# Kernel tuning notes

Hardware: AMD Instinct MI355X
Metric: run time of the kernel (lower is better)

Reference implementation:

```python
import jax, jax.numpy as jnp
import numpy as np

N_TOKENS = 8192
EMBED = 1024
HIDDEN = 4 * EMBED
NUM_EXPERTS = 8


def setup_inputs() -> dict:
    key = jax.random.key(0)
    ks = jax.random.split(key, 10)
    s = 0.02
    return {
        "x": jax.random.normal(ks[0], (N_TOKENS, EMBED), dtype=jnp.float32),
        # Router params
        "Wr1": jax.random.normal(ks[1], (EMBED, EMBED), dtype=jnp.float32) * s,
        "br1": jnp.zeros((EMBED,), dtype=jnp.float32),
        "Wr2": jax.random.normal(ks[2], (EMBED, NUM_EXPERTS), dtype=jnp.float32) * s,
        "br2": jnp.zeros((NUM_EXPERTS,), dtype=jnp.float32),
        # Expert FFN params, stacked over experts
        "W1": jax.random.normal(ks[3], (NUM_EXPERTS, EMBED, HIDDEN), dtype=jnp.float32) * s,
        "b1": jnp.zeros((NUM_EXPERTS, HIDDEN), dtype=jnp.float32),
        "W2": jax.random.normal(ks[4], (NUM_EXPERTS, HIDDEN, EMBED), dtype=jnp.float32) * s,
        "b2": jnp.zeros((NUM_EXPERTS, EMBED), dtype=jnp.float32),
    }


def reference(x, Wr1, br1, Wr2, br2, W1, b1, W2, b2):
    # Router: Linear -> ReLU -> Linear -> softmax over experts -> top-1
    h = jax.nn.relu(x @ Wr1 + br1)                      # [N, E]
    probs = jax.nn.softmax(h @ Wr2 + br2, axis=1)       # [N, num_experts]
    chosen = jnp.argmax(probs, axis=1)                  # [N]

    num_experts = W1.shape[0]
    out = jnp.zeros_like(x)
    # Fixed small loop over experts (structurally distinct weights).
    for e in range(num_experts):
        ffn_e = jax.nn.relu(x @ W1[e] + b1[e]) @ W2[e] + b2[e]  # [N, E]
        out = jnp.where((chosen == e)[:, None], ffn_e, out)
    # Note: original returns raw expert output (no probability weighting).
    return out
```

## Files before the change

kernel.cpp:

```cpp
#include <hip/hip_runtime.h>
#include <stdint.h>

#define N_TOK 8192
#define EMB 1024
#define HID 4096
#define NEXP 8

typedef _Float16 f16x8 __attribute__((ext_vector_type(8)));
typedef _Float16 f16x4 __attribute__((ext_vector_type(4)));
typedef short    s16x8 __attribute__((ext_vector_type(8)));
typedef unsigned short u16x8 __attribute__((ext_vector_type(8)));
typedef float    f32x4 __attribute__((ext_vector_type(4)));

typedef __attribute__((address_space(1))) const void gvoid_t;
typedef __attribute__((address_space(3))) void lvoid_t;

__device__ __forceinline__ void async16(const void* g, void* l) {
  __builtin_amdgcn_global_load_lds((gvoid_t*)g, (lvoid_t*)l, 16, 0, 0);
}

__device__ __forceinline__ unsigned short f2bf(float f) {
  unsigned u = __builtin_bit_cast(unsigned, f);
  u += 0x7fffu + ((u >> 16) & 1u);
  return (unsigned short)(u >> 16);
}

__global__ __launch_bounds__(256) void k_cast_x(const float* __restrict__ x,
    unsigned short* __restrict__ xb, _Float16* __restrict__ xhi, _Float16* __restrict__ xlo) {
  int i = (blockIdx.x * 256 + threadIdx.x) << 2;
  float4 v = *(const float4*)(x + i);
  ushort4 b;
  b.x = f2bf(v.x); b.y = f2bf(v.y); b.z = f2bf(v.z); b.w = f2bf(v.w);
  *(ushort4*)(xb + i) = b;
  float vv[4] = {v.x, v.y, v.z, v.w};
  f16x4 hi, lo;
#pragma unroll
  for (int j = 0; j < 4; j++) {
    _Float16 h = (_Float16)vv[j];
    hi[j] = h;
    lo[j] = (_Float16)(vv[j] - (float)h);
  }
  *(f16x4*)(xhi + i) = hi;
  *(f16x4*)(xlo + i) = lo;
}

__global__ __launch_bounds__(256) void k_trans_wr1(const float* __restrict__ src,
    _Float16* __restrict__ dhi, _Float16* __restrict__ dlo) {
  int nblk = blockIdx.x >> 4, kc = blockIdx.x & 15;
  int n = (nblk << 8) + threadIdx.x;
  int k0 = kc << 6;
  for (int k = k0; k < k0 + 64; k += 8) {
    f16x8 hi, lo;
#pragma unroll
    for (int j = 0; j < 8; j++) {
      float w = src[(size_t)(k + j) * EMB + n] * 256.0f;
      _Float16 h = (_Float16)w;
      hi[j] = h;
      lo[j] = (_Float16)(w - (float)h);
    }
    *(f16x8*)(dhi + (size_t)n * EMB + k) = hi;
    *(f16x8*)(dlo + (size_t)n * EMB + k) = lo;
  }
}

__global__ __launch_bounds__(256) void k_transcast_v2(const float* __restrict__ src,
    unsigned short* __restrict__ dst, int K, int Nn, int ktiles, int ntiles) {
  __shared__ __align__(16) unsigned short lds[256 * 72];
  int b = blockIdx.x;
  int e = b / (ktiles * ntiles);
  int r = b % (ktiles * ntiles);
  int kt = r / ntiles, nt = r % ntiles;
  int k0 = kt << 6, n0 = nt << 8;
  const float* s = src + (size_t)e * K * Nn;
  unsigned short* d = dst + (size_t)e * K * Nn;
  int tid = threadIdx.x;
  const float* scol = s + n0 + tid;
#pragma unroll 4
  for (int k = 0; k < 64; k += 2) {
    float a  = scol[(size_t)(k0 + k) * Nn];
    float bv = scol[(size_t)(k0 + k + 1) * Nn];
    unsigned p = (unsigned)f2bf(a) | ((unsigned)f2bf(bv) << 16);
    *(unsigned*)(lds + tid * 72 + k) = p;
  }
  __syncthreads();
  int c = tid & 7, nl = tid >> 3;
#pragma unroll
  for (int p2 = 0; p2 < 8; p2++) {
    int n = (p2 << 5) + nl;
    u16x8 v = *(const u16x8*)(lds + n * 72 + (c << 3));
    *(u16x8*)(d + (size_t)(n0 + n) * K + k0 + (c << 3)) = v;
  }
}

__global__ __launch_bounds__(256) void k_router_gemm(
    const _Float16* __restrict__ Ah, const _Float16* __restrict__ Al,
    const _Float16* __restrict__ Bh, const _Float16* __restrict__ Bl,
    const float* __restrict__ br1, float* __restrict__ hOut) {
  __shared__ __align__(16) _Float16 sAh[4096], sAl[4096], sBh[4096], sBl[4096];
  const int tid = threadIdx.x, lane = tid & 63, wave = tid >> 6;
  const int m0 = (blockIdx.x >> 3) << 7;
  const int n0 = (blockIdx.x & 7) << 7;
  const int srow = (wave << 5) + (lane >> 2);
  const int scol = (lane & 3) << 3;
  const size_t aBase = (size_t)(m0 + srow) * EMB + scol;
  const size_t bBase = (size_t)(n0 + srow) * EMB + scol;
  _Float16* lAh = sAh + (wave << 10);
  _Float16* lAl = sAl + (wave << 10);
  _Float16* lBh = sBh + (wave << 10);
  _Float16* lBl = sBl + (wave << 10);
  const int q = lane >> 4, c = lane & 15;
  const int msub = (wave & 1) << 6, nsub = (wave >> 1) << 6;
  f32x4 acc[4][4];
#pragma unroll
  for (int i = 0; i < 4; i++)
#pragma unroll
    for (int j = 0; j < 4; j++) acc[i][j] = (f32x4){0.f, 0.f, 0.f, 0.f};

  for (int kk = 0; kk < EMB; kk += 32) {
    async16(Ah + aBase + kk, lAh);
    async16(Ah + aBase + 16 * EMB + kk, lAh + 512);
    async16(Al + aBase + kk, lAl);
    async16(Al + aBase + 16 * EMB + kk, lAl + 512);
    async16(Bh + bBase + kk, lBh);
    async16(Bh + bBase + 16 * EMB + kk, lBh + 512);
    async16(Bl + bBase + kk, lBl);
    async16(Bl + bBase + 16 * EMB + kk, lBl + 512);
    __syncthreads();
    f16x8 fah[4], fal[4], fbh[4], fbl[4];
#pragma unroll
    for (int i = 0; i < 4; i++) {
      int ar = msub + (i << 4) + c;
      int br = nsub + (i << 4) + c;
      fah[i] = *(const f16x8*)(sAh + (ar << 5) + (q << 3));
      fal[i] = *(const f16x8*)(sAl + (ar << 5) + (q << 3));
      fbh[i] = *(const f16x8*)(sBh + (br << 5) + (q << 3));
      fbl[i] = *(const f16x8*)(sBl + (br << 5) + (q << 3));
    }
#pragma unroll
    for (int mi = 0; mi < 4; mi++)
#pragma unroll
      for (int ni = 0; ni < 4; ni++) {
        acc[mi][ni] = __builtin_amdgcn_mfma_f32_16x16x32_f16(fah[mi], fbh[ni], acc[mi][ni], 0, 0, 0);
        acc[mi][ni] = __builtin_amdgcn_mfma_f32_16x16x32_f16(fah[mi], fbl[ni], acc[mi][ni], 0, 0, 0);
        acc[mi][ni] = __builtin_amdgcn_mfma_f32_16x16x32_f16(fal[mi], fbh[ni], acc[mi][ni], 0, 0, 0);
      }
    __syncthreads();
  }
#pragma unroll
  for (int mi = 0; mi < 4; mi++)
#pragma unroll
    for (int ni = 0; ni < 4; ni++) {
      int gn = n0 + nsub + (ni << 4) + c;
      float bias = 256.0f * br1[gn];
#pragma unroll
      for (int i2 = 0; i2 < 4; i2++) {
        int gm = m0 + msub + (mi << 4) + (q << 2) + i2;
        float v = acc[mi][ni][i2] + bias;
        hOut[(size_t)gm * EMB + gn] = v > 0.f ? v : 0.f;
      }
    }
}

__global__ __launch_bounds__(256) void k_logits(const float* __restrict__ h,
    const float* __restrict__ Wr2, const float* __restrict__ br2, int* __restrict__ chosen) {
  __shared__ __align__(16) float sW[EMB * NEXP];
  int tid = threadIdx.x;
  for (int i = tid; i < EMB * NEXP; i += 256) sW[i] = Wr2[i];
  __syncthreads();
  int lane = tid & 63, wave = tid >> 6;
  int t = blockIdx.x * 4 + wave;
  const float* hr = h + (size_t)t * EMB;
  float acc[8] = {0.f, 0.f, 0.f, 0.f, 0.f, 0.f, 0.f, 0.f};
#pragma unroll
  for (int i = 0; i < 16; i++) {
    int k = (i << 6) + lane;
    float v = hr[k];
    float4 w0 = *(const float4*)(sW + (k << 3));
    float4 w1 = *(const float4*)(sW + (k << 3) + 4);
    acc[0] += v * w0.x; acc[1] += v * w0.y; acc[2] += v * w0.z; acc[3] += v * w0.w;
    acc[4] += v * w1.x; acc[5] += v * w1.y; acc[6] += v * w1.z; acc[7] += v * w1.w;
  }
#pragma unroll
  for (int off = 32; off > 0; off >>= 1)
#pragma unroll
    for (int e = 0; e < 8; e++) acc[e] += __shfl_down(acc[e], off);
  if (lane == 0) {
    float best = acc[0] + 256.0f * br2[0];
    int bi = 0;
#pragma unroll
    for (int e = 1; e < 8; e++) {
      float l = acc[e] + 256.0f * br2[e];
      if (l > best) { best = l; bi = e; }
    }
    chosen[t] = bi;
  }
}

__global__ void k_zero(int* meta) { meta[threadIdx.x] = 0; }

__global__ __launch_bounds__(256) void k_hist(const int* __restrict__ chosen, int* meta) {
  int i = blockIdx.x * 256 + threadIdx.x;
  atomicAdd(&meta[chosen[i]], 1);
}

__global__ __launch_bounds__(128) void k_sched(int* meta) {
  __shared__ int cnt[8];
  int tid = threadIdx.x;
  if (tid < 8) cnt[tid] = meta[tid];
  __syncthreads();
  int off[9]; off[0] = 0;
#pragma unroll
  for (int e = 0; e < 8; e++) off[e + 1] = off[e] + cnt[e];
  if (tid < 8) meta[16 + tid] = off[tid];
  int ts[9]; ts[0] = 0;
#pragma unroll
  for (int e = 0; e < 8; e++) ts[e + 1] = ts[e] + ((cnt[e] + 127) >> 7);
  int T = ts[8];
  if (tid == 0) { meta[24] = off[8]; meta[25] = T; }
  if (tid < T) {
    int e = 0;
    while (ts[e + 1] <= tid) e++;
    int m = off[e] + ((tid - ts[e]) << 7);
    int end = off[e + 1];
    meta[32 + tid] = e;
    meta[112 + tid] = m;
    meta[192 + tid] = (m + 128 < end) ? m + 128 : end;
  }
  int ts2[9]; ts2[0] = 0;
#pragma unroll
  for (int e = 0; e < 8; e++) ts2[e + 1] = ts2[e] + ((cnt[e] + 255) >> 8);
  int T2 = ts2[8];
  if (tid == 0) meta[26] = T2;
  if (tid < T2) {
    int e = 0;
    while (ts2[e + 1] <= tid) e++;
    int m = off[e] + ((tid - ts2[e]) << 8);
    int end = off[e + 1];
    meta[288 + tid] = e;
    meta[368 + tid] = m;
    meta[448 + tid] = (m + 256 < end) ? m + 256 : end;
  }
}

__global__ __launch_bounds__(256) void k_scatter(const int* __restrict__ chosen,
                                                 int* meta, int* __restrict__ perm) {
  int i = blockIdx.x * 256 + threadIdx.x;
  int e = chosen[i];
  int pos = meta[16 + e] + atomicAdd(&meta[8 + e], 1);
  perm[pos] = i;
}

__global__ __launch_bounds__(512) void k_ffn1(
    const unsigned short* __restrict__ xb, const unsigned short* __restrict__ w1t,
    const float* __restrict__ b1, const int* __restrict__ perm,
    const int* __restrict__ meta, unsigned short* __restrict__ hidden) {
  const int wg = (blockIdx.x & 7) * 160 + (blockIdx.x >> 3);
  const int mt = wg >> 5;
  if (mt >= meta[26]) return;
  const int nt = wg & 31;
  const int e = meta[288 + mt];
  const int row0 = meta[368 + mt];
  const int rend = meta[448 + mt];
  const int n0 = nt << 7;
  __shared__ __align__(16) unsigned short sA[256 * 64], sB[128 * 64];
  const int tid = threadIdx.x, lane = tid & 63, wave = tid >> 6;
  const int lr = lane >> 3;
  const int scol = ((lane & 7) ^ lr) << 3;
  const unsigned short* aptr[4];
#pragma unroll
  for (int j = 0; j < 4; j++) {
    int r = row0 + (wave << 5) + (j << 3) + lr;
    if (r > N_TOK - 1) r = N_TOK - 1;
    aptr[j] = xb + (size_t)perm[r] * EMB + scol;
  }
  const unsigned short* bptr[2];
#pragma unroll
  for (int j = 0; j < 2; j++) {
    int r = n0 + (wave << 4) + (j << 3) + lr;
    bptr[j] = w1t + (size_t)e * EMB * HID + (size_t)r * EMB + scol;
  }
  const int q = lane >> 4, c = lane & 15;
  const int msub = (wave >> 1) << 6;
  const int nsub = (wave & 1) << 6;
  f32x4 acc[4][4];
#pragma unroll
  for (int i = 0; i < 4; i++)
#pragma unroll
    for (int j = 0; j < 4; j++) acc[i][j] = (f32x4){0.f, 0.f, 0.f, 0.f};

#pragma unroll 1
  for (int kk = 0; kk < EMB; kk += 64) {
    async16(aptr[0] + kk, sA + ((wave << 5) + 0)  * 64);
    async16(aptr[1] + kk, sA + ((wave << 5) + 8)  * 64);
    async16(aptr[2] + kk, sA + ((wave << 5) + 16) * 64);
    async16(aptr[3] + kk, sA + ((wave << 5) + 24) * 64);
    async16(bptr[0] + kk, sB + ((wave << 4) + 0)  * 64);
    async16(bptr[1] + kk, sB + ((wave << 4) + 8)  * 64);
    __syncthreads();
#pragma unroll
    for (int ks = 0; ks < 2; ks++) {
      const int coff = ((((ks << 2) + q) ^ (c & 7)) << 3);
      s16x8 fa[4], fb[4];
#pragma unroll
      for (int i = 0; i < 4; i++) {
        fa[i] = *(const s16x8*)(sA + ((msub + (i << 4) + c) << 6) + coff);
        fb[i] = *(const s16x8*)(sB + ((nsub + (i << 4) + c) << 6) + coff);
      }
#pragma unroll
      for (int mi = 0; mi < 4; mi++)
#pragma unroll
        for (int ni = 0; ni < 4; ni++)
          acc[mi][ni] = __builtin_amdgcn_mfma_f32_16x16x32_bf16(fa[mi], fb[ni], acc[mi][ni], 0, 0, 0);
    }
    __syncthreads();
  }
#pragma unroll
  for (int mi = 0; mi < 4; mi++)
#pragma unroll
    for (int ni = 0; ni < 4; ni++) {
      int gn = n0 + nsub + (ni << 4) + c;
      float bias = b1[e * HID + gn];
#pragma unroll
      for (int i2 = 0; i2 < 4; i2++) {
        int rs = row0 + msub + (mi << 4) + (q << 2) + i2;
        if (rs < rend) {
          float v = acc[mi][ni][i2] + bias;
          v = v > 0.f ? v : 0.f;
          hidden[(size_t)rs * HID + gn] = f2bf(v);
        }
      }
    }
}

__global__ __launch_bounds__(512) void k_ffn2(
    const unsigned short* __restrict__ hidden, const unsigned short* __restrict__ w2t,
    const float* __restrict__ b2, const int* __restrict__ perm,
    const int* __restrict__ meta, float* __restrict__ out) {
  const int wg = (blockIdx.x & 7) * 40 + (blockIdx.x >> 3);
  const int mt = wg >> 3;
  if (mt >= meta[26]) return;
  const int nt = wg & 7;
  const int e = meta[288 + mt];
  const int row0 = meta[368 + mt];
  const int rend = meta[448 + mt];
  const int n0 = nt << 7;
  __shared__ __align__(16) unsigned short sA[256 * 64], sB[128 * 64];
  const int tid = threadIdx.x, lane = tid & 63, wave = tid >> 6;
  const int lr = lane >> 3;
  const int scol = ((lane & 7) ^ lr) << 3;
  const unsigned short* aptr[4];
#pragma unroll
  for (int j = 0; j < 4; j++) {
    int r = row0 + (wave << 5) + (j << 3) + lr;
    if (r > N_TOK - 1) r = N_TOK - 1;
    aptr[j] = hidden + (size_t)r * HID + scol;
  }
  const unsigned short* bptr[2];
#pragma unroll
  for (int j = 0; j < 2; j++) {
    int r = n0 + (wave << 4) + (j << 3) + lr;
    bptr[j] = w2t + (size_t)e * HID * EMB + (size_t)r * HID + scol;
  }
  const int q = lane >> 4, c = lane & 15;
  const int msub = (wave >> 1) << 6;
  const int nsub = (wave & 1) << 6;
  f32x4 acc[4][4];
#pragma unroll
  for (int i = 0; i < 4; i++)
#pragma unroll
    for (int j = 0; j < 4; j++) acc[i][j] = (f32x4){0.f, 0.f, 0.f, 0.f};

#pragma unroll 1
  for (int kk = 0; kk < HID; kk += 64) {
    async16(aptr[0] + kk, sA + ((wave << 5) + 0)  * 64);
    async16(aptr[1] + kk, sA + ((wave << 5) + 8)  * 64);
    async16(aptr[2] + kk, sA + ((wave << 5) + 16) * 64);
    async16(aptr[3] + kk, sA + ((wave << 5) + 24) * 64);
    async16(bptr[0] + kk, sB + ((wave << 4) + 0)  * 64);
    async16(bptr[1] + kk, sB + ((wave << 4) + 8)  * 64);
    __syncthreads();
#pragma unroll
    for (int ks = 0; ks < 2; ks++) {
      const int coff = ((((ks << 2) + q) ^ (c & 7)) << 3);
      s16x8 fa[4], fb[4];
#pragma unroll
      for (int i = 0; i < 4; i++) {
        fa[i] = *(const s16x8*)(sA + ((msub + (i << 4) + c) << 6) + coff);
        fb[i] = *(const s16x8*)(sB + ((nsub + (i << 4) + c) << 6) + coff);
      }
#pragma unroll
      for (int mi = 0; mi < 4; mi++)
#pragma unroll
        for (int ni = 0; ni < 4; ni++)
          acc[mi][ni] = __builtin_amdgcn_mfma_f32_16x16x32_bf16(fa[mi], fb[ni], acc[mi][ni], 0, 0, 0);
    }
    __syncthreads();
  }
#pragma unroll
  for (int mi = 0; mi < 4; mi++)
#pragma unroll
    for (int ni = 0; ni < 4; ni++) {
      int gn = n0 + nsub + (ni << 4) + c;
      float bias = b2[e * EMB + gn];
#pragma unroll
      for (int i2 = 0; i2 < 4; i2++) {
        int rs = row0 + msub + (mi << 4) + (q << 2) + i2;
        if (rs < rend) {
          int orig = perm[rs];
          out[(size_t)orig * EMB + gn] = acc[mi][ni][i2] + bias;
        }
      }
    }
}

extern "C" void kernel_launch(void* const* d_in, const int* in_sizes, int n_in,
                              void* d_out, int out_size, void* d_ws, size_t ws_size,
                              hipStream_t stream) {
  const float* x   = (const float*)d_in[0];
  const float* Wr1 = (const float*)d_in[1];
  const float* br1 = (const float*)d_in[2];
  const float* Wr2 = (const float*)d_in[3];
  const float* br2 = (const float*)d_in[4];
  const float* W1  = (const float*)d_in[5];
  const float* b1  = (const float*)d_in[6];
  const float* W2  = (const float*)d_in[7];
  const float* b2  = (const float*)d_in[8];
  float* out = (float*)d_out;
  char* ws = (char*)d_ws;

  unsigned short* w1t    = (unsigned short*)(ws + 0);
  unsigned short* w2t    = (unsigned short*)(ws + 67108864);
  unsigned short* xb     = (unsigned short*)(ws + 134217728);
  _Float16*       xhi    = (_Float16*)(ws + 150994944);
  _Float16*       xlo    = (_Float16*)(ws + 167772160);
  _Float16*       whi    = (_Float16*)(ws + 184549376);
  _Float16*       wlo    = (_Float16*)(ws + 186646528);
  float*          hbuf   = (float*)(ws + 188743680);
  unsigned short* hidden = (unsigned short*)(ws + 222298112);
  int*            chosen = (int*)(ws + 289406976);
  int*            perm   = (int*)(ws + 289439744);
  int*            meta   = (int*)(ws + 289472512);

  k_cast_x<<<dim3(8192), dim3(256), 0, stream>>>(x, xb, xhi, xlo);
  k_trans_wr1<<<dim3(64), dim3(256), 0, stream>>>(Wr1, whi, wlo);
  k_transcast_v2<<<dim3(2048), dim3(256), 0, stream>>>(W1, w1t, 1024, 4096, 16, 16);
  k_transcast_v2<<<dim3(2048), dim3(256), 0, stream>>>(W2, w2t, 4096, 1024, 64, 4);
  k_router_gemm<<<dim3(512), dim3(256), 0, stream>>>(xhi, xlo, whi, wlo, br1, hbuf);
  k_logits<<<dim3(2048), dim3(256), 0, stream>>>(hbuf, Wr2, br2, chosen);
  k_zero<<<dim3(1), dim3(256), 0, stream>>>(meta);
  k_hist<<<dim3(32), dim3(256), 0, stream>>>(chosen, meta);
  k_sched<<<dim3(1), dim3(128), 0, stream>>>(meta);
  k_scatter<<<dim3(32), dim3(256), 0, stream>>>(chosen, meta, perm);
  k_ffn1<<<dim3(1280), dim3(512), 0, stream>>>(xb, w1t, b1, perm, meta, hidden);
  k_ffn2<<<dim3(320), dim3(512), 0, stream>>>(hidden, w2t, b2, perm, meta, out);
}
```

Baseline: 777.6 us.

## Split-K the second expert GEMM and merge routing kernels into one

The second expert FFN GEMM is split into two K-halves, launching twice as many workgroups. Each half writes fp32 partial sums to scratch buffers, and a new reduce kernel adds them, applies the bias and scatters rows back to their original token order. This is meant to fix the poor CU fill of the previous 320-block launch, at the cost of extra partial-sum traffic and one more launch. The four routing kernels (zero, histogram, schedule, scatter) are also merged into one single-block kernel using LDS atomics, cutting launch overhead.

```diff
diff --git a/kernel.cpp b/kernel.cpp
--- a/kernel.cpp
+++ b/kernel.cpp
@@ -196,36 +196,18 @@
   }
 }
 
-__global__ void k_zero(int* meta) { meta[threadIdx.x] = 0; }
-
-__global__ __launch_bounds__(256) void k_hist(const int* __restrict__ chosen, int* meta) {
-  int i = blockIdx.x * 256 + threadIdx.x;
-  atomicAdd(&meta[chosen[i]], 1);
-}
-
-__global__ __launch_bounds__(128) void k_sched(int* meta) {
-  __shared__ int cnt[8];
+__global__ __launch_bounds__(256) void k_route(const int* __restrict__ chosen,
+                                               int* meta, int* __restrict__ perm) {
+  __shared__ int cnt[8], cur[8];
   int tid = threadIdx.x;
-  if (tid < 8) cnt[tid] = meta[tid];
+  if (tid < 8) { cnt[tid] = 0; cur[tid] = 0; }
+  __syncthreads();
+  for (int i = tid; i < N_TOK; i += 256) atomicAdd(&cnt[chosen[i]], 1);
   __syncthreads();
   int off[9]; off[0] = 0;
 #pragma unroll
   for (int e = 0; e < 8; e++) off[e + 1] = off[e] + cnt[e];
   if (tid < 8) meta[16 + tid] = off[tid];
-  int ts[9]; ts[0] = 0;
-#pragma unroll
-  for (int e = 0; e < 8; e++) ts[e + 1] = ts[e] + ((cnt[e] + 127) >> 7);
-  int T = ts[8];
-  if (tid == 0) { meta[24] = off[8]; meta[25] = T; }
-  if (tid < T) {
-    int e = 0;
-    while (ts[e + 1] <= tid) e++;
-    int m = off[e] + ((tid - ts[e]) << 7);
-    int end = off[e + 1];
-    meta[32 + tid] = e;
-    meta[112 + tid] = m;
-    meta[192 + tid] = (m + 128 < end) ? m + 128 : end;
-  }
   int ts2[9]; ts2[0] = 0;
 #pragma unroll
   for (int e = 0; e < 8; e++) ts2[e + 1] = ts2[e] + ((cnt[e] + 255) >> 8);
@@ -240,14 +222,11 @@
     meta[368 + tid] = m;
     meta[448 + tid] = (m + 256 < end) ? m + 256 : end;
   }
-}
-
-__global__ __launch_bounds__(256) void k_scatter(const int* __restrict__ chosen,
-                                                 int* meta, int* __restrict__ perm) {
-  int i = blockIdx.x * 256 + threadIdx.x;
-  int e = chosen[i];
-  int pos = meta[16 + e] + atomicAdd(&meta[8 + e], 1);
-  perm[pos] = i;
+  for (int i = tid; i < N_TOK; i += 256) {
+    int e = chosen[i];
+    int pos = off[e] + atomicAdd(&cur[e], 1);
+    perm[pos] = i;
+  }
 }
 
 __global__ __launch_bounds__(512) void k_ffn1(
@@ -334,16 +313,18 @@
 
 __global__ __launch_bounds__(512) void k_ffn2(
     const unsigned short* __restrict__ hidden, const unsigned short* __restrict__ w2t,
-    const float* __restrict__ b2, const int* __restrict__ perm,
-    const int* __restrict__ meta, float* __restrict__ out) {
-  const int wg = (blockIdx.x & 7) * 40 + (blockIdx.x >> 3);
-  const int mt = wg >> 3;
+    const int* __restrict__ meta, float* __restrict__ p0, float* __restrict__ p1) {
+  const int wg = (blockIdx.x & 7) * 80 + (blockIdx.x >> 3);
+  const int kc = wg / 320;
+  const int r  = wg % 320;
+  const int mt = r >> 3;
   if (mt >= meta[26]) return;
-  const int nt = wg & 7;
+  const int nt = r & 7;
   const int e = meta[288 + mt];
   const int row0 = meta[368 + mt];
   const int rend = meta[448 + mt];
   const int n0 = nt << 7;
+  const int kbase = kc << 11;
   __shared__ __align__(16) unsigned short sA[256 * 64], sB[128 * 64];
   const int tid = threadIdx.x, lane = tid & 63, wave = tid >> 6;
   const int lr = lane >> 3;
@@ -351,15 +332,15 @@
   const unsigned short* aptr[4];
 #pragma unroll
   for (int j = 0; j < 4; j++) {
-    int r = row0 + (wave << 5) + (j << 3) + lr;
-    if (r > N_TOK - 1) r = N_TOK - 1;
-    aptr[j] = hidden + (size_t)r * HID + scol;
+    int rr = row0 + (wave << 5) + (j << 3) + lr;
+    if (rr > N_TOK - 1) rr = N_TOK - 1;
+    aptr[j] = hidden + (size_t)rr * HID + kbase + scol;
   }
   const unsigned short* bptr[2];
 #pragma unroll
   for (int j = 0; j < 2; j++) {
-    int r = n0 + (wave << 4) + (j << 3) + lr;
-    bptr[j] = w2t + (size_t)e * HID * EMB + (size_t)r * HID + scol;
+    int rr = n0 + (wave << 4) + (j << 3) + lr;
+    bptr[j] = w2t + (size_t)e * HID * EMB + (size_t)rr * HID + kbase + scol;
   }
   const int q = lane >> 4, c = lane & 15;
   const int msub = (wave >> 1) << 6;
@@ -371,7 +352,7 @@
     for (int j = 0; j < 4; j++) acc[i][j] = (f32x4){0.f, 0.f, 0.f, 0.f};
 
 #pragma unroll 1
-  for (int kk = 0; kk < HID; kk += 64) {
+  for (int kk = 0; kk < 2048; kk += 64) {
     async16(aptr[0] + kk, sA + ((wave << 5) + 0)  * 64);
     async16(aptr[1] + kk, sA + ((wave << 5) + 8)  * 64);
     async16(aptr[2] + kk, sA + ((wave << 5) + 16) * 64);
@@ -396,21 +377,38 @@
     }
     __syncthreads();
   }
+  float* pout = kc ? p1 : p0;
 #pragma unroll
   for (int mi = 0; mi < 4; mi++)
 #pragma unroll
     for (int ni = 0; ni < 4; ni++) {
       int gn = n0 + nsub + (ni << 4) + c;
-      float bias = b2[e * EMB + gn];
 #pragma unroll
       for (int i2 = 0; i2 < 4; i2++) {
         int rs = row0 + msub + (mi << 4) + (q << 2) + i2;
-        if (rs < rend) {
-          int orig = perm[rs];
-          out[(size_t)orig * EMB + gn] = acc[mi][ni][i2] + bias;
-        }
-      }
-    }
+        if (rs < rend) pout[((size_t)rs << 10) + gn] = acc[mi][ni][i2];
+      }
+    }
+}
+
+__global__ __launch_bounds__(256) void k_reduce(
+    const float* __restrict__ p0, const float* __restrict__ p1,
+    const float* __restrict__ b2, const int* __restrict__ perm,
+    const int* __restrict__ chosen, float* __restrict__ out) {
+  int rs = blockIdx.x;
+  int n = threadIdx.x << 2;
+  int orig = perm[rs];
+  int e = chosen[orig];
+  size_t idx = ((size_t)rs << 10) + n;
+  float4 a = *(const float4*)(p0 + idx);
+  float4 b = *(const float4*)(p1 + idx);
+  float4 bb = *(const float4*)(b2 + e * EMB + n);
+  float4 rv;
+  rv.x = a.x + b.x + bb.x;
+  rv.y = a.y + b.y + bb.y;
+  rv.z = a.z + b.z + bb.z;
+  rv.w = a.w + b.w + bb.w;
+  *(float4*)(out + ((size_t)orig << 10) + n) = rv;
 }
 
 extern "C" void kernel_launch(void* const* d_in, const int* in_sizes, int n_in,
@@ -440,6 +438,8 @@
   int*            chosen = (int*)(ws + 289406976);
   int*            perm   = (int*)(ws + 289439744);
   int*            meta   = (int*)(ws + 289472512);
+  float*          p0     = (float*)(ws + 0);
+  float*          p1     = (float*)(ws + 33554432);
 
   k_cast_x<<<dim3(8192), dim3(256), 0, stream>>>(x, xb, xhi, xlo);
   k_trans_wr1<<<dim3(64), dim3(256), 0, stream>>>(Wr1, whi, wlo);
@@ -447,10 +447,8 @@
   k_transcast_v2<<<dim3(2048), dim3(256), 0, stream>>>(W2, w2t, 4096, 1024, 64, 4);
   k_router_gemm<<<dim3(512), dim3(256), 0, stream>>>(xhi, xlo, whi, wlo, br1, hbuf);
   k_logits<<<dim3(2048), dim3(256), 0, stream>>>(hbuf, Wr2, br2, chosen);
-  k_zero<<<dim3(1), dim3(256), 0, stream>>>(meta);
-  k_hist<<<dim3(32), dim3(256), 0, stream>>>(chosen, meta);
-  k_sched<<<dim3(1), dim3(128), 0, stream>>>(meta);
-  k_scatter<<<dim3(32), dim3(256), 0, stream>>>(chosen, meta, perm);
+  k_route<<<dim3(1), dim3(256), 0, stream>>>(chosen, meta, perm);
   k_ffn1<<<dim3(1280), dim3(512), 0, stream>>>(xb, w1t, b1, perm, meta, hidden);
-  k_ffn2<<<dim3(320), dim3(512), 0, stream>>>(hidden, w2t, b2, perm, meta, out);
-}
+  k_ffn2<<<dim3(640), dim3(512), 0, stream>>>(hidden, w2t, meta, p0, p1);
+  k_reduce<<<dim3(8192), dim3(256), 0, stream>>>(p0, p1, b2, perm, chosen, out);
+}
```

Measured after the change: 695.5 us. -10.6%, faster.
